# Kernel optimization log

Hardware: AMD Instinct MI355X
Metric: run time of the kernel (lower is better)

## Reference

```python
import jax, jax.numpy as jnp
import numpy as np

N = 100000
E = 1600000
C_IN, C_HID, C_OUT = 128, 256, 128
EPS = 1e-5


def glorot(key, fan_in, fan_out):
    lim = np.sqrt(6.0 / (fan_in + fan_out))
    return jax.random.uniform(key, (fan_in, fan_out), jnp.float32, -lim, lim)


def setup_inputs() -> dict:
    key = jax.random.key(0)
    ks = jax.random.split(key, 6)
    x = jax.random.normal(ks[0], (N, C_IN), jnp.float32)
    edge_index = jax.random.randint(ks[1], (2, E), 0, N, jnp.int64)
    W1 = glorot(ks[2], C_IN, C_HID)
    b1 = jnp.zeros((C_HID,), jnp.float32)
    W2 = glorot(ks[3], C_HID, C_OUT)
    b2 = jnp.zeros((C_OUT,), jnp.float32)
    gamma = jnp.ones((C_OUT,), jnp.float32)
    beta = jnp.zeros((C_OUT,), jnp.float32)
    return {"x": x, "edge_index": edge_index, "W1": W1, "b1": b1,
            "W2": W2, "b2": b2, "gamma": gamma, "beta": beta}


def gcn_conv(x, src, dst, W, b, n):
    # linear transform first (PyG GCNConv), then normalized scatter-add aggregation
    h = x @ W  # [N, C_out]
    loops = jnp.arange(n, dtype=src.dtype)
    src2 = jnp.concatenate([src, loops])  # self-loops added
    dst2 = jnp.concatenate([dst, loops])
    ones = jnp.ones(src2.shape, h.dtype)
    deg = jax.ops.segment_sum(ones, dst2, num_segments=n)  # in-degree incl. self-loop
    dinv = jax.lax.rsqrt(deg)  # deg >= 1 thanks to self-loops
    coeff = dinv[src2] * dinv[dst2]  # symmetric normalization per edge
    msgs = h[src2] * coeff[:, None]  # [E+N, C_out] gathered messages
    out = jax.ops.segment_sum(msgs, dst2, num_segments=n)
    return out + b


def layer_norm(x, gamma, beta):
    mu = jnp.mean(x, axis=-1, keepdims=True)
    var = jnp.mean(jnp.square(x - mu), axis=-1, keepdims=True)
    return (x - mu) * jax.lax.rsqrt(var + EPS) * gamma + beta


def reference(x, edge_index, W1, b1, W2, b2, gamma, beta):
    src, dst = edge_index[0], edge_index[1]
    h = gcn_conv(x, src, dst, W1, b1, N)
    h = jax.nn.relu(h)
    h = gcn_conv(h, src, dst, W2, b2, N)
    return layer_norm(h, gamma, beta)
```

## Files before the change

kernel.cpp:

```cpp
#include <hip/hip_runtime.h>
#include <hip/hip_bf16.h>

#define C_IN  128
#define C_HID 256
#define C_OUT 128

#define BIN_SHIFT 10
#define BIN_SIZE  1024
#define NBINS_MAX 128
#define CAP       32768
#define CHUNK_A   8192

typedef __attribute__((ext_vector_type(8))) short short8;
typedef __attribute__((ext_vector_type(4))) float f32x4;

static __device__ __forceinline__ unsigned short f2bf(float f) {
    __hip_bfloat16 h = __float2bfloat16(f);
    return __builtin_bit_cast(unsigned short, h);
}
static __device__ __forceinline__ float bf2f(unsigned short u) {
    unsigned int x = ((unsigned int)u) << 16;
    return __builtin_bit_cast(float, x);
}

static __device__ __forceinline__ void pack_one(const float* __restrict__ W,
                                                unsigned short* __restrict__ Wp,
                                                int o, int NKS, int M) {
    int j    = o & 7;
    int lane = (o >> 3) & 63;
    int rest = o >> 9;
    int ks = rest % NKS;
    int ct = rest / NKS;
    int k = ks * 32 + (lane >> 4) * 8 + j;
    int m = ct * 16 + (lane & 15);
    Wp[o] = f2bf(W[(size_t)k * M + m]);
}

#define CVT_BLOCKS   512
#define PACK_BLOCKS  128

__global__ __launch_bounds__(256) void prep_kernel(const float* __restrict__ x,
                                                   unsigned short* __restrict__ x16, int n4,
                                                   const float* __restrict__ W1,
                                                   unsigned short* __restrict__ w1p,
                                                   const float* __restrict__ W2,
                                                   unsigned short* __restrict__ w2p,
                                                   const int* __restrict__ src,
                                                   const int* __restrict__ dst,
                                                   unsigned int* __restrict__ binned,
                                                   int* __restrict__ gbin_cnt,
                                                   int e, int n) {
    __shared__ int lh[NBINS_MAX];
    __shared__ int lgb[NBINS_MAX];
    __shared__ int lh2[NBINS_MAX];
    const int b = blockIdx.x, tid = threadIdx.x;
    if (b < CVT_BLOCKS) {
        for (int i = b * 256 + tid; i < n4; i += CVT_BLOCKS * 256) {
            float4 v = *(const float4*)&x[(size_t)i * 4];
            ushort4 o;
            o.x = f2bf(v.x); o.y = f2bf(v.y); o.z = f2bf(v.z); o.w = f2bf(v.w);
            *(ushort4*)&x16[(size_t)i * 4] = o;
        }
    } else if (b < CVT_BLOCKS + PACK_BLOCKS) {
        pack_one(W1, w1p, (b - CVT_BLOCKS) * 256 + tid, C_IN / 32, C_HID);
    } else if (b < CVT_BLOCKS + 2 * PACK_BLOCKS) {
        pack_one(W2, w2p, (b - CVT_BLOCKS - PACK_BLOCKS) * 256 + tid, C_HID / 32, C_OUT);
    } else {
        const int cb = b - CVT_BLOCKS - 2 * PACK_BLOCKS;
        const int start = cb * CHUNK_A;
        const int end = min(start + CHUNK_A, e);
        const int nbins = (n + BIN_SIZE - 1) >> BIN_SHIFT;
        for (int j = tid; j < nbins; j += 256) { lh[j] = 0; lh2[j] = 0; }
        __syncthreads();
        for (int i = start + tid; i < end; i += 256) {
            unsigned d = (unsigned)dst[i], s = (unsigned)src[i];
            if (d < (unsigned)n && s < (unsigned)n)
                atomicAdd(&lh[d >> BIN_SHIFT], 1);
        }
        __syncthreads();
        for (int j = tid; j < nbins; j += 256) {
            int c = lh[j];
            lgb[j] = c ? atomicAdd(&gbin_cnt[j], c) : 0;
        }
        __syncthreads();
        for (int i = start + tid; i < end; i += 256) {
            unsigned d = (unsigned)dst[i], s = (unsigned)src[i];
            if (d < (unsigned)n && s < (unsigned)n) {
                int bin = d >> BIN_SHIFT;
                int r = atomicAdd(&lh2[bin], 1);
                int pos = lgb[bin] + r;
                if (pos < CAP)
                    binned[(size_t)bin * CAP + pos] = (s << BIN_SHIFT) | (d & (BIN_SIZE - 1));
            }
        }
    }
}

__global__ __launch_bounds__(1024) void binscan_kernel(const int* __restrict__ gbin_cnt,
                                                       int* __restrict__ bin_base,
                                                       int* __restrict__ row_start,
                                                       int nbins, int n) {
    const int tid = threadIdx.x, lane = tid & 63, w = tid >> 6;
    int v = (tid < nbins) ? gbin_cnt[tid] : 0;
    int x = v;
    #pragma unroll
    for (int off = 1; off < 64; off <<= 1) {
        int y = __shfl_up(x, off);
        if (lane >= off) x += y;
    }
    __shared__ int ws[16];
    if (lane == 63) ws[w] = x;
    __syncthreads();
    int woff = 0, total = 0;
    #pragma unroll
    for (int j = 0; j < 16; ++j) {
        int s = ws[j];
        if (j < w) woff += s;
        total += s;
    }
    if (tid < nbins) bin_base[tid] = woff + (x - v);
    if (tid == 0) { bin_base[nbins] = total; row_start[n] = total; }
}

__global__ __launch_bounds__(1024) void bincsr_kernel(const unsigned int* __restrict__ binned,
                                                      const int* __restrict__ bin_base,
                                                      int* __restrict__ csr_src,
                                                      int* __restrict__ row_start,
                                                      float* __restrict__ dinv, int n) {
    __shared__ int h[BIN_SIZE];
    __shared__ int ex[BIN_SIZE];
    __shared__ int ws[16];
    const int b = blockIdx.x, tid = threadIdx.x, lane = tid & 63, w = tid >> 6;
    h[tid] = 0;
    __syncthreads();
    const int base  = bin_base[b];
    int cnt_b = bin_base[b + 1] - base;
    if (cnt_b > CAP) cnt_b = CAP;
    const size_t boff = (size_t)b * CAP;
    for (int i = tid; i < cnt_b; i += BIN_SIZE)
        atomicAdd(&h[binned[boff + i] & (BIN_SIZE - 1)], 1);
    __syncthreads();
    const int v = h[tid];
    int x = v;
    #pragma unroll
    for (int off = 1; off < 64; off <<= 1) {
        int y = __shfl_up(x, off);
        if (lane >= off) x += y;
    }
    if (lane == 63) ws[w] = x;
    __syncthreads();
    int woff = 0;
    #pragma unroll
    for (int j = 0; j < 16; ++j)
        if (j < w) woff += ws[j];
    const int excl = woff + (x - v);
    ex[tid] = excl;
    const int node = b * BIN_SIZE + tid;
    if (node < n) {
        row_start[node] = base + excl;
        dinv[node] = rsqrtf((float)(v + 1));
    }
    __syncthreads();
    h[tid] = 0;
    __syncthreads();
    for (int i = tid; i < cnt_b; i += BIN_SIZE) {
        unsigned p = binned[boff + i];
        int dl = p & (BIN_SIZE - 1);
        int r = atomicAdd(&h[dl], 1);
        csr_src[base + ex[dl] + r] = (int)(p >> BIN_SHIFT);
    }
}

template<int K, int M, bool BIASRELU>
__global__ __launch_bounds__(256) void gemm_mfma_kernel(const unsigned short* __restrict__ A,
                                                        const unsigned short* __restrict__ Wp,
                                                        unsigned short* __restrict__ C,
                                                        const float* __restrict__ bias, int n) {
    constexpr int NKS = K / 32;
    constexpr int NCT = M / 16;
    __shared__ unsigned short wl[K * M];
    const int tid  = threadIdx.x;
    const int lane = tid & 63;
    const int wid  = tid >> 6;

    for (int i = tid; i < K * M / 8; i += 256)
        *(uint4*)&wl[(size_t)i * 8] = *(const uint4*)&Wp[(size_t)i * 8];
    __syncthreads();

    const int ntiles = (n + 63) / 64;
    for (int t = blockIdx.x; t < ntiles; t += gridDim.x) {
        const int row0 = t * 64 + wid * 16;
        int arow = row0 + (lane & 15);
        if (arow > n - 1) arow = n - 1;
        const unsigned short* ap = A + (size_t)arow * K + (lane >> 4) * 8;

        short8 afrag[NKS];
        #pragma unroll
        for (int ks = 0; ks < NKS; ++ks)
            afrag[ks] = *(const short8*)(ap + ks * 32);

        f32x4 acc[NCT] = {};
        #pragma unroll
        for (int ks = 0; ks < NKS; ++ks) {
            #pragma unroll
            for (int ct = 0; ct < NCT; ++ct) {
                short8 b = *(const short8*)&wl[((ct * NKS + ks) * 64 + lane) * 8];
                acc[ct] = __builtin_amdgcn_mfma_f32_16x16x32_bf16(afrag[ks], b, acc[ct], 0, 0, 0);
            }
        }

        const int crow0 = row0 + (lane >> 4) * 4;
        const int ccol  = lane & 15;
        #pragma unroll
        for (int ct = 0; ct < NCT; ++ct) {
            float bv = BIASRELU ? bias[ct * 16 + ccol] : 0.f;
            #pragma unroll
            for (int r = 0; r < 4; ++r) {
                int row = crow0 + r;
                if (row < n) {
                    float v = acc[ct][r];
                    if (BIASRELU) v = fmaxf(v + bv, 0.f);
                    C[(size_t)row * M + ct * 16 + ccol] = f2bf(v);
                }
            }
        }
    }
}

template<int CH, int NPW, bool HASBIAS, bool RELU, bool LN>
__global__ __launch_bounds__(256) void agg_kernel(const unsigned short* __restrict__ H,
                                                  const int* __restrict__ row_start,
                                                  const int* __restrict__ csr_src,
                                                  const float* __restrict__ dinv,
                                                  const float* __restrict__ bias,
                                                  const float* __restrict__ gamma,
                                                  const float* __restrict__ beta,
                                                  void* __restrict__ out_v, int n) {
    constexpr int SUBW = 64 / NPW;
    static_assert(CH == SUBW * 4, "layout");
    const int lane = threadIdx.x & 63;
    const int wid  = threadIdx.x >> 6;
    int node = blockIdx.x * 4 * NPW + wid * NPW + (NPW == 2 ? (lane >> 5) : 0);
    if (NPW == 1) node = __builtin_amdgcn_readfirstlane(node);
    if (node >= n) return;
    const int slane = lane & (SUBW - 1);
    const int c0 = slane * 4;

    const float dn = dinv[node];
    const int e0 = row_start[node], e1 = row_start[node + 1];

    float acc[4];
    {
        float c = dn * dn;
        ushort4 h = *(const ushort4*)&H[(size_t)node * CH + c0];
        acc[0] = bf2f(h.x) * c; acc[1] = bf2f(h.y) * c;
        acc[2] = bf2f(h.z) * c; acc[3] = bf2f(h.w) * c;
    }
    int e = e0;
    for (; e + 4 <= e1; e += 4) {
        int s0 = csr_src[e + 0], s1 = csr_src[e + 1];
        int s2 = csr_src[e + 2], s3 = csr_src[e + 3];
        float w0 = dinv[s0] * dn, w1 = dinv[s1] * dn;
        float w2 = dinv[s2] * dn, w3 = dinv[s3] * dn;
        ushort4 h0 = *(const ushort4*)&H[(size_t)s0 * CH + c0];
        ushort4 h1 = *(const ushort4*)&H[(size_t)s1 * CH + c0];
        ushort4 h2 = *(const ushort4*)&H[(size_t)s2 * CH + c0];
        ushort4 h3 = *(const ushort4*)&H[(size_t)s3 * CH + c0];
        acc[0] += bf2f(h0.x) * w0; acc[1] += bf2f(h0.y) * w0;
        acc[2] += bf2f(h0.z) * w0; acc[3] += bf2f(h0.w) * w0;
        acc[0] += bf2f(h1.x) * w1; acc[1] += bf2f(h1.y) * w1;
        acc[2] += bf2f(h1.z) * w1; acc[3] += bf2f(h1.w) * w1;
        acc[0] += bf2f(h2.x) * w2; acc[1] += bf2f(h2.y) * w2;
        acc[2] += bf2f(h2.z) * w2; acc[3] += bf2f(h2.w) * w2;
        acc[0] += bf2f(h3.x) * w3; acc[1] += bf2f(h3.y) * w3;
        acc[2] += bf2f(h3.z) * w3; acc[3] += bf2f(h3.w) * w3;
    }
    for (; e < e1; ++e) {
        int s = csr_src[e];
        float c = dinv[s] * dn;
        ushort4 h = *(const ushort4*)&H[(size_t)s * CH + c0];
        acc[0] += bf2f(h.x) * c; acc[1] += bf2f(h.y) * c;
        acc[2] += bf2f(h.z) * c; acc[3] += bf2f(h.w) * c;
    }

    if (HASBIAS) {
        float4 bi = *(const float4*)&bias[c0];
        acc[0] += bi.x; acc[1] += bi.y; acc[2] += bi.z; acc[3] += bi.w;
    }
    if (RELU) {
        #pragma unroll
        for (int v = 0; v < 4; ++v) acc[v] = fmaxf(acc[v], 0.f);
    }

    if (LN) {
        float s = acc[0] + acc[1] + acc[2] + acc[3];
        float ss = acc[0]*acc[0] + acc[1]*acc[1] + acc[2]*acc[2] + acc[3]*acc[3];
        #pragma unroll
        for (int off = SUBW / 2; off; off >>= 1) {
            s  += __shfl_xor(s, off);
            ss += __shfl_xor(ss, off);
        }
        float mu  = s * (1.f / (float)CH);
        float var = ss * (1.f / (float)CH) - mu * mu;
        float rstd = rsqrtf(var + 1e-5f);
        float4 g = *(const float4*)&gamma[c0];
        float4 b = *(const float4*)&beta[c0];
        f32x4 o;
        o[0] = (acc[0] - mu) * rstd * g.x + b.x;
        o[1] = (acc[1] - mu) * rstd * g.y + b.y;
        o[2] = (acc[2] - mu) * rstd * g.z + b.z;
        o[3] = (acc[3] - mu) * rstd * g.w + b.w;
        float* out = (float*)out_v;
        __builtin_nontemporal_store(o, (f32x4*)&out[(size_t)node * CH + c0]);
    } else {
        ushort4 o4;
        o4.x = f2bf(acc[0]); o4.y = f2bf(acc[1]);
        o4.z = f2bf(acc[2]); o4.w = f2bf(acc[3]);
        unsigned short* out = (unsigned short*)out_v;
        *(ushort4*)&out[(size_t)node * CH + c0] = o4;
    }
}

extern "C" void kernel_launch(void* const* d_in, const int* in_sizes, int n_in,
                              void* d_out, int out_size, void* d_ws, size_t ws_size,
                              hipStream_t stream) {
    const float* x     = (const float*)d_in[0];
    const int*   ei    = (const int*)d_in[1];
    const float* W1    = (const float*)d_in[2];
    const float* b1    = (const float*)d_in[3];
    const float* W2    = (const float*)d_in[4];
    const float* b2    = (const float*)d_in[5];
    const float* gamma = (const float*)d_in[6];
    const float* beta  = (const float*)d_in[7];
    float* out = (float*)d_out;

    const int N = in_sizes[0] / C_IN;
    const int E = in_sizes[1] / 2;
    const int* src = ei;
    const int* dst = ei + E;
    const int NBINS = (N + BIN_SIZE - 1) >> BIN_SHIFT;
    const int NBINA = (E + CHUNK_A - 1) / CHUNK_A;

    unsigned short* x16 = (unsigned short*)d_ws;
    unsigned short* xa  = x16 + (size_t)N * C_IN;
    unsigned short* g16 = xa + (size_t)N * C_IN;
    unsigned short* h2  = g16 + (size_t)N * C_HID;
    unsigned short* w1p = h2 + (size_t)N * C_OUT;
    unsigned short* w2p = w1p + C_IN * C_HID;
    float* dinv  = (float*)(w2p + C_HID * C_OUT);
    int*   row_start = (int*)(dinv + N);
    int*   gbin_cnt  = row_start + N + 4;
    int*   bin_base  = gbin_cnt + NBINS_MAX;
    unsigned int* binned = (unsigned int*)(bin_base + NBINS_MAX + 4);
    int*   csr_src   = (int*)(binned + (size_t)NBINS_MAX * CAP);

    hipMemsetAsync(gbin_cnt, 0, NBINS_MAX * sizeof(int), stream);

    prep_kernel<<<CVT_BLOCKS + 2 * PACK_BLOCKS + NBINA, 256, 0, stream>>>(
        x, x16, N * C_IN / 4, W1, w1p, W2, w2p, src, dst, binned, gbin_cnt, E, N);
    binscan_kernel<<<1, 1024, 0, stream>>>(gbin_cnt, bin_base, row_start, NBINS, N);
    bincsr_kernel<<<NBINS, 1024, 0, stream>>>(binned, bin_base, csr_src, row_start, dinv, N);

    agg_kernel<C_IN, 2, false, false, false><<<(N + 7) / 8, 256, 0, stream>>>(
        x16, row_start, csr_src, dinv, nullptr, nullptr, nullptr, (void*)xa, N);
    gemm_mfma_kernel<C_IN, C_HID, true><<<512, 256, 0, stream>>>(xa, w1p, g16, b1, N);

    gemm_mfma_kernel<C_HID, C_OUT, false><<<512, 256, 0, stream>>>(g16, w2p, h2, nullptr, N);
    agg_kernel<C_OUT, 2, true, false, true><<<(N + 7) / 8, 256, 0, stream>>>(
        h2, row_start, csr_src, dinv, b2, gamma, beta, (void*)out, N);
}
```

Before: 264.8 us.

## Quantize input features to per-row int8 for first-layer aggregation gather

```diff
diff --git a/kernel.cpp b/kernel.cpp
--- a/kernel.cpp
+++ b/kernel.cpp
@@ -40,7 +40,8 @@
 #define PACK_BLOCKS  128
 
 __global__ __launch_bounds__(256) void prep_kernel(const float* __restrict__ x,
-                                                   unsigned short* __restrict__ x16, int n4,
+                                                   unsigned char* __restrict__ xq,
+                                                   float* __restrict__ xscale,
                                                    const float* __restrict__ W1,
                                                    unsigned short* __restrict__ w1p,
                                                    const float* __restrict__ W2,
@@ -55,11 +56,20 @@
     __shared__ int lh2[NBINS_MAX];
     const int b = blockIdx.x, tid = threadIdx.x;
     if (b < CVT_BLOCKS) {
-        for (int i = b * 256 + tid; i < n4; i += CVT_BLOCKS * 256) {
-            float4 v = *(const float4*)&x[(size_t)i * 4];
-            ushort4 o;
-            o.x = f2bf(v.x); o.y = f2bf(v.y); o.z = f2bf(v.z); o.w = f2bf(v.w);
-            *(ushort4*)&x16[(size_t)i * 4] = o;
+        const int slane = tid & 31;
+        const int subrow = tid >> 5;
+        for (int row = b * 8 + subrow; row < n; row += CVT_BLOCKS * 8) {
+            float4 v = *(const float4*)&x[(size_t)row * C_IN + slane * 4];
+            float m = fmaxf(fmaxf(fabsf(v.x), fabsf(v.y)), fmaxf(fabsf(v.z), fabsf(v.w)));
+            #pragma unroll
+            for (int off = 16; off; off >>= 1) m = fmaxf(m, __shfl_xor(m, off));
+            float inv = (m > 0.f) ? 127.f / m : 0.f;
+            int q0 = (int)rintf(v.x * inv), q1 = (int)rintf(v.y * inv);
+            int q2 = (int)rintf(v.z * inv), q3 = (int)rintf(v.w * inv);
+            unsigned int p = ((unsigned)q0 & 0xff) | (((unsigned)q1 & 0xff) << 8) |
+                             (((unsigned)q2 & 0xff) << 16) | (((unsigned)q3 & 0xff) << 24);
+            *(unsigned int*)&xq[(size_t)row * C_IN + slane * 4] = p;
+            if (slane == 0) xscale[row] = m * (1.f / 127.f);
         }
     } else if (b < CVT_BLOCKS + PACK_BLOCKS) {
         pack_one(W1, w1p, (b - CVT_BLOCKS) * 256 + tid, C_IN / 32, C_HID);
@@ -124,9 +134,11 @@
 
 __global__ __launch_bounds__(1024) void bincsr_kernel(const unsigned int* __restrict__ binned,
                                                       const int* __restrict__ bin_base,
+                                                      const float* __restrict__ xscale,
                                                       int* __restrict__ csr_src,
                                                       int* __restrict__ row_start,
-                                                      float* __restrict__ dinv, int n) {
+                                                      float* __restrict__ dinv,
+                                                      float* __restrict__ dscale, int n) {
     __shared__ int h[BIN_SIZE];
     __shared__ int ex[BIN_SIZE];
     __shared__ int ws[16];
@@ -158,7 +170,9 @@
     const int node = b * BIN_SIZE + tid;
     if (node < n) {
         row_start[node] = base + excl;
-        dinv[node] = rsqrtf((float)(v + 1));
+        float di = rsqrtf((float)(v + 1));
+        dinv[node] = di;
+        dscale[node] = di * xscale[node];
     }
     __syncthreads();
     h[tid] = 0;
@@ -227,69 +241,75 @@
     }
 }
 
-template<int CH, int NPW, bool HASBIAS, bool RELU, bool LN>
-__global__ __launch_bounds__(256) void agg_kernel(const unsigned short* __restrict__ H,
+template<int CH, bool INT8IN, bool HASBIAS, bool LN>
+__global__ __launch_bounds__(256) void agg_kernel(const void* __restrict__ H_v,
                                                   const int* __restrict__ row_start,
                                                   const int* __restrict__ csr_src,
                                                   const float* __restrict__ dinv,
+                                                  const float* __restrict__ cw,
                                                   const float* __restrict__ bias,
                                                   const float* __restrict__ gamma,
                                                   const float* __restrict__ beta,
                                                   void* __restrict__ out_v, int n) {
-    constexpr int SUBW = 64 / NPW;
+    constexpr int SUBW = 32;
     static_assert(CH == SUBW * 4, "layout");
     const int lane = threadIdx.x & 63;
     const int wid  = threadIdx.x >> 6;
-    int node = blockIdx.x * 4 * NPW + wid * NPW + (NPW == 2 ? (lane >> 5) : 0);
-    if (NPW == 1) node = __builtin_amdgcn_readfirstlane(node);
+    int node = blockIdx.x * 8 + wid * 2 + (lane >> 5);
     if (node >= n) return;
     const int slane = lane & (SUBW - 1);
     const int c0 = slane * 4;
 
+    const unsigned char*  H8  = (const unsigned char*)H_v;
+    const unsigned short* H16 = (const unsigned short*)H_v;
+
     const float dn = dinv[node];
     const int e0 = row_start[node], e1 = row_start[node + 1];
 
     float acc[4];
+    #define LOAD4(sidx, v0, v1, v2, v3)                                             \
+        float v0, v1, v2, v3;                                                       \
+        if (INT8IN) {                                                               \
+            unsigned int p = *(const unsigned int*)&H8[(size_t)(sidx) * CH + c0];   \
+            v0 = (float)(int)(signed char)(p & 0xff);                               \
+            v1 = (float)(int)(signed char)((p >> 8) & 0xff);                        \
+            v2 = (float)(int)(signed char)((p >> 16) & 0xff);                       \
+            v3 = (float)(int)(signed char)(p >> 24);                                \
+        } else {                                                                    \
+            ushort4 hh = *(const ushort4*)&H16[(size_t)(sidx) * CH + c0];           \
+            v0 = bf2f(hh.x); v1 = bf2f(hh.y); v2 = bf2f(hh.z); v3 = bf2f(hh.w);     \
+        }
     {
-        float c = dn * dn;
-        ushort4 h = *(const ushort4*)&H[(size_t)node * CH + c0];
-        acc[0] = bf2f(h.x) * c; acc[1] = bf2f(h.y) * c;
-        acc[2] = bf2f(h.z) * c; acc[3] = bf2f(h.w) * c;
+        float c = dn * cw[node];
+        LOAD4(node, h0, h1, h2, h3)
+        acc[0] = h0 * c; acc[1] = h1 * c; acc[2] = h2 * c; acc[3] = h3 * c;
     }
     int e = e0;
     for (; e + 4 <= e1; e += 4) {
         int s0 = csr_src[e + 0], s1 = csr_src[e + 1];
         int s2 = csr_src[e + 2], s3 = csr_src[e + 3];
-        float w0 = dinv[s0] * dn, w1 = dinv[s1] * dn;
-        float w2 = dinv[s2] * dn, w3 = dinv[s3] * dn;
-        ushort4 h0 = *(const ushort4*)&H[(size_t)s0 * CH + c0];
-        ushort4 h1 = *(const ushort4*)&H[(size_t)s1 * CH + c0];
-        ushort4 h2 = *(const ushort4*)&H[(size_t)s2 * CH + c0];
-        ushort4 h3 = *(const ushort4*)&H[(size_t)s3 * CH + c0];
-        acc[0] += bf2f(h0.x) * w0; acc[1] += bf2f(h0.y) * w0;
-        acc[2] += bf2f(h0.z) * w0; acc[3] += bf2f(h0.w) * w0;
-        acc[0] += bf2f(h1.x) * w1; acc[1] += bf2f(h1.y) * w1;
-        acc[2] += bf2f(h1.z) * w1; acc[3] += bf2f(h1.w) * w1;
-        acc[0] += bf2f(h2.x) * w2; acc[1] += bf2f(h2.y) * w2;
-        acc[2] += bf2f(h2.z) * w2; acc[3] += bf2f(h2.w) * w2;
-        acc[0] += bf2f(h3.x) * w3; acc[1] += bf2f(h3.y) * w3;
-        acc[2] += bf2f(h3.z) * w3; acc[3] += bf2f(h3.w) * w3;
+        float w0 = cw[s0] * dn, w1 = cw[s1] * dn;
+        float w2 = cw[s2] * dn, w3 = cw[s3] * dn;
+        LOAD4(s0, a0, a1, a2, a3)
+        LOAD4(s1, b0, b1, b2, b3)
+        LOAD4(s2, c0v, c1v, c2v, c3v)
+        LOAD4(s3, d0, d1, d2, d3)
+        acc[0] += a0 * w0;  acc[1] += a1 * w0;  acc[2] += a2 * w0;  acc[3] += a3 * w0;
+        acc[0] += b0 * w1;  acc[1] += b1 * w1;  acc[2] += b2 * w1;  acc[3] += b3 * w1;
+        acc[0] += c0v * w2; acc[1] += c1v * w2; acc[2] += c2v * w2; acc[3] += c3v * w2;
+        acc[0] += d0 * w3;  acc[1] += d1 * w3;  acc[2] += d2 * w3;  acc[3] += d3 * w3;
     }
     for (; e < e1; ++e) {
         int s = csr_src[e];
-        float c = dinv[s] * dn;
-        ushort4 h = *(const ushort4*)&H[(size_t)s * CH + c0];
-        acc[0] += bf2f(h.x) * c; acc[1] += bf2f(h.y) * c;
-        acc[2] += bf2f(h.z) * c; acc[3] += bf2f(h.w) * c;
-    }
+        float c = cw[s] * dn;
+        LOAD4(s, h0, h1, h2, h3)
+        acc[0] += h0 * c; acc[1] += h1 * c; acc[2] += h2 * c; acc[3] += h3 * c;
+    }
+    #undef LOAD4
 
     if (HASBIAS) {
         float4 bi = *(const float4*)&bias[c0];
         acc[0] += bi.x; acc[1] += bi.y; acc[2] += bi.z; acc[3] += bi.w;
-    }
-    if (RELU) {
-        #pragma unroll
-        for (int v = 0; v < 4; ++v) acc[v] = fmaxf(acc[v], 0.f);
     }
 
     if (LN) {
@@ -341,14 +361,16 @@
     const int NBINS = (N + BIN_SIZE - 1) >> BIN_SHIFT;
     const int NBINA = (E + CHUNK_A - 1) / CHUNK_A;
 
-    unsigned short* x16 = (unsigned short*)d_ws;
-    unsigned short* xa  = x16 + (size_t)N * C_IN;
+    unsigned char*  xq  = (unsigned char*)d_ws;
+    unsigned short* xa  = (unsigned short*)(xq + (size_t)N * C_IN);
     unsigned short* g16 = xa + (size_t)N * C_IN;
     unsigned short* h2  = g16 + (size_t)N * C_HID;
     unsigned short* w1p = h2 + (size_t)N * C_OUT;
     unsigned short* w2p = w1p + C_IN * C_HID;
-    float* dinv  = (float*)(w2p + C_HID * C_OUT);
-    int*   row_start = (int*)(dinv + N);
+    float* dinv   = (float*)(w2p + C_HID * C_OUT);
+    float* dscale = dinv + N;
+    float* xscale = dscale + N;
+    int*   row_start = (int*)(xscale + N);
     int*   gbin_cnt  = row_start + N + 4;
     int*   bin_base  = gbin_cnt + NBINS_MAX;
     unsigned int* binned = (unsigned int*)(bin_base + NBINS_MAX + 4);
@@ -357,15 +379,17 @@
     hipMemsetAsync(gbin_cnt, 0, NBINS_MAX * sizeof(int), stream);
 
     prep_kernel<<<CVT_BLOCKS + 2 * PACK_BLOCKS + NBINA, 256, 0, stream>>>(
-        x, x16, N * C_IN / 4, W1, w1p, W2, w2p, src, dst, binned, gbin_cnt, E, N);
+        x, xq, xscale, W1, w1p, W2, w2p, src, dst, binned, gbin_cnt, E, N);
     binscan_kernel<<<1, 1024, 0, stream>>>(gbin_cnt, bin_base, row_start, NBINS, N);
-    bincsr_kernel<<<NBINS, 1024, 0, stream>>>(binned, bin_base, csr_src, row_start, dinv, N);
-
-    agg_kernel<C_IN, 2, false, false, false><<<(N + 7) / 8, 256, 0, stream>>>(
-        x16, row_start, csr_src, dinv, nullptr, nullptr, nullptr, (void*)xa, N);
+    bincsr_kernel<<<NBINS, 1024, 0, stream>>>(binned, bin_base, xscale,
+                                              csr_src, row_start, dinv, dscale, N);
+
+    agg_kernel<C_IN, true, false, false><<<(N + 7) / 8, 256, 0, stream>>>(
+        (const void*)xq, row_start, csr_src, dinv, dscale,
+        nullptr, nullptr, nullptr, (void*)xa, N);
     gemm_mfma_kernel<C_IN, C_HID, true><<<512, 256, 0, stream>>>(xa, w1p, g16, b1, N);
 
     gemm_mfma_kernel<C_HID, C_OUT, false><<<512, 256, 0, stream>>>(g16, w2p, h2, nullptr, N);
-    agg_kernel<C_OUT, 2, true, false, true><<<(N + 7) / 8, 256, 0, stream>>>(
-        h2, row_start, csr_src, dinv, b2, gamma, beta, (void*)out, N);
-}
+    agg_kernel<C_OUT, false, true, true><<<(N + 7) / 8, 256, 0, stream>>>(
+        (const void*)h2, row_start, csr_src, dinv, dinv, b2, gamma, beta, (void*)out, N);
+}
```

Result: faster. 245.5 us (-7.3%).
